# Performance work log

Hardware: AMD Instinct MI355X
Metric: run time of the kernel (lower is better)

The kernel has to match this reference:

```python
import jax, jax.numpy as jnp
import numpy as np

M0, M1 = 16, 8            # scalar / vector multiplicities of node_irreps (16x0e + 8x1o)
N_NODES = 10000
N_EDGES = 160000
H_EDGE = 64
W_NUMEL = M0*M0 + M1*M0 + M0*M1 + M1*M1  # 576 per-edge TP weights
EPS = 1e-5


def setup_inputs() -> dict:
    key = jax.random.key(0)
    ks = jax.random.split(key, 8)
    return {
        "node_features": jax.random.normal(ks[0], (N_NODES, M0 + 3*M1), jnp.float32),
        "edge_features": jax.random.normal(ks[1], (N_EDGES, H_EDGE), jnp.float32),
        "edge_sh": jax.random.normal(ks[2], (N_EDGES, 4), jnp.float32),
        "edge_index": jax.random.randint(ks[3], (2, N_EDGES), 0, N_NODES),
        "fc_w1": jax.random.normal(ks[4], (H_EDGE, H_EDGE), jnp.float32) / np.sqrt(H_EDGE),
        "fc_b1": jnp.zeros((H_EDGE,), jnp.float32),
        "fc_w2": jax.random.normal(ks[5], (H_EDGE, W_NUMEL), jnp.float32) / np.sqrt(H_EDGE),
        "fc_b2": jnp.zeros((W_NUMEL,), jnp.float32),
        "bn_w_s": jnp.ones((M0,), jnp.float32),
        "bn_b_s": jnp.zeros((M0,), jnp.float32),
        "bn_w_v": jnp.ones((M1,), jnp.float32),
    }


def reference(node_features, edge_features, edge_sh, edge_index,
              fc_w1, fc_b1, fc_w2, fc_b2, bn_w_s, bn_b_s, bn_w_v):
    N = node_features.shape[0]
    E = edge_features.shape[0]
    edge_dst, edge_src = edge_index[0], edge_index[1]

    # per-edge TP weights from a small MLP on edge features
    w = jax.nn.relu(edge_features @ fc_w1 + fc_b1) @ fc_w2 + fc_b2  # [E, 576]

    # gather node features on destination side
    x = node_features[edge_dst]                      # [E, 40]
    x0 = x[:, :M0]                                   # [E, 16] scalars (0e)
    x1 = x[:, M0:].reshape(E, M1, 3)                 # [E, 8, 3] vectors (1o)
    sh0 = edge_sh[:, 0]                              # [E] l=0
    sh1 = edge_sh[:, 1:4]                            # [E, 3] l=1

    # split per-edge weights by tensor-product path
    o1 = M0*M0; o2 = o1 + M1*M0; o3 = o2 + M0*M1
    w00 = w[:, :o1].reshape(E, M0, M0)               # 0e x 0e -> 0e
    w11 = w[:, o1:o2].reshape(E, M1, M0)             # 1o x 1o -> 0e
    w01 = w[:, o2:o3].reshape(E, M0, M1)             # 0e x 1o -> 1o
    w10 = w[:, o3:].reshape(E, M1, M1)               # 1o x 0e -> 1o

    inv3 = 1.0 / np.sqrt(3.0)                        # w3j(1,1,0) coefficient
    alpha = 1.0 / np.sqrt(M0 + M1)                   # path fan-in normalization

    out0 = (jnp.einsum('eu,euv->ev', x0 * sh0[:, None], w00)
            + inv3 * jnp.einsum('eui,ei,euv->ev', x1, sh1, w11)) * alpha   # [E, 16]
    out1 = (jnp.einsum('eu,ei,euv->evi', x0, sh1, w01)
            + jnp.einsum('e,eui,euv->evi', sh0, x1, w10)) * alpha          # [E, 8, 3]

    tp = jnp.concatenate([out0, out1.reshape(E, 3*M1)], axis=-1)           # [E, 40]

    # scatter_mean over source nodes
    seg = jax.ops.segment_sum(tp, edge_src, num_segments=N)                # [N, 40]
    cnt = jax.ops.segment_sum(jnp.ones((E, 1), tp.dtype), edge_src, num_segments=N)
    out = seg / jnp.maximum(cnt, 1.0)

    # residual (pad is zero-width since tp output irreps == node irreps)
    out = out + node_features

    # e3nn-style BatchNorm (training mode, component normalization)
    s = out[:, :M0]
    v = out[:, M0:].reshape(N, M1, 3)
    mu = s.mean(axis=0)
    s = s - mu
    var = (s * s).mean(axis=0)
    s = s * (jax.lax.rsqrt(var + EPS) * bn_w_s) + bn_b_s
    vnorm = (v * v).mean(axis=-1).mean(axis=0)       # [M1]
    v = v * (jax.lax.rsqrt(vnorm + EPS) * bn_w_v)[None, :, None]
    out = jnp.concatenate([s, v.reshape(N, 3*M1)], axis=-1)

    return out, edge_features
```

## Files before the change

### kernel.cpp

```cpp
#include <hip/hip_runtime.h>

typedef __attribute__((ext_vector_type(8))) short short8;
typedef __attribute__((ext_vector_type(4))) float f32x4;
typedef __attribute__((ext_vector_type(4))) ushort u16x4;

constexpr int NN = 10000;
constexpr int NE = 160000;
constexpr int NT = NE / 16;
constexpr int TPSTR = 48;
constexpr int GBLK = 625;
constexpr float EPSV = 1e-5f;
constexpr float INV3 = 0.57735026918962576f;
constexpr float ALPHA = 0.20412414523193152f;

__device__ __forceinline__ ushort f2bf(float x) {
  unsigned u = __float_as_uint(x);
  u += 0x7fffu + ((u >> 16) & 1u);
  return (ushort)(u >> 16);
}
__device__ __forceinline__ float bf2f(ushort u) {
  return __uint_as_float(((unsigned)u) << 16);
}
__device__ __forceinline__ f32x4 mfma16(short8 a, short8 b, f32x4 c) {
  return __builtin_amdgcn_mfma_f32_16x16x32_bf16(a, b, c, 0, 0, 0);
}

template <typename T> struct TPS;
template <> struct TPS<float> {
  static __device__ __forceinline__ void st4(float* p, f32x4 v) { *(f32x4*)p = v; }
  static __device__ __forceinline__ float ld(const float* p) { return *p; }
};
template <> struct TPS<ushort> {
  static __device__ __forceinline__ void st4(ushort* p, f32x4 v) {
    u16x4 o;
#pragma unroll
    for (int j = 0; j < 4; ++j) o[j] = f2bf(v[j]);
    *(u16x4*)p = o;
  }
  static __device__ __forceinline__ float ld(const ushort* p) { return bf2f(*p); }
};

constexpr int PREP_DEGB = (NN + 63) / 64;
__global__ __launch_bounds__(64) void prep_w2(const float* __restrict__ w2,
                                              short8* __restrict__ w2bf,
                                              int* __restrict__ deg,
                                              const float* __restrict__ b2,
                                              float* __restrict__ flag) {
  int b = blockIdx.x;
  int lane = threadIdx.x;
  if (b < 72) {
    int jt = b >> 1, kc = b & 1;
    int g = lane >> 4, c = lane & 15;
    short8 v;
#pragma unroll
    for (int j = 0; j < 8; ++j)
      v[j] = (short)f2bf(w2[(kc * 32 + 8 * g + j) * 576 + jt * 16 + c]);
    w2bf[(jt * 2 + kc) * 64 + lane] = v;
  } else if (b < 72 + PREP_DEGB) {
    int idx = (b - 72) * 64 + lane;
    if (idx < NN) deg[idx] = 0;
  } else {
    float m = 0.f;
    for (int i = lane; i < 576; i += 64) m = fmaxf(m, fabsf(b2[i]));
#pragma unroll
    for (int off = 1; off < 64; off <<= 1) m = fmaxf(m, __shfl_xor(m, off));
    if (lane == 0) *flag = m;
  }
}

constexpr int CSTR = 68;
constexpr unsigned SM_W2 = 4608 * 16;
constexpr unsigned SM_B2 = 576 * 4;
constexpr unsigned SM_W1 = 512 * 16;
constexpr unsigned SM_B1 = 64 * 4;
constexpr unsigned SM_HL = 8 * 16 * 72 * 2;
constexpr unsigned SM_SCR = 8 * 16 * CSTR * 4;
constexpr unsigned SM_TOTAL = SM_W2 + SM_B2 + SM_W1 + SM_B1 + SM_HL + SM_SCR;

template <typename T>
__global__ __launch_bounds__(512) void conv_kernel(
    const float* __restrict__ ef, const float* __restrict__ w1,
    const float* __restrict__ b1, const short8* __restrict__ w2bf,
    const float* __restrict__ b2, const float* __restrict__ nf,
    const float* __restrict__ sh, const int* __restrict__ ei,
    const int* __restrict__ perm, float* __restrict__ efout, int do_copy,
    T* __restrict__ tp, const float* __restrict__ flagp)
{
  extern __shared__ char smem[];
  short8* w2lds = (short8*)smem;
  float*  b2lds = (float*)(smem + SM_W2);
  short8* w1f   = (short8*)(smem + SM_W2 + SM_B2);
  float*  b1lds = (float*)(smem + SM_W2 + SM_B2 + SM_W1);
  ushort* hlall = (ushort*)(smem + SM_W2 + SM_B2 + SM_W1 + SM_B1);
  float*  scrall = (float*)(smem + SM_W2 + SM_B2 + SM_W1 + SM_B1 + SM_HL);

  const int tid = threadIdx.x;
  for (int i = tid; i < 4608; i += 512) w2lds[i] = w2bf[i];
  for (int i = tid; i < 576; i += 512) b2lds[i] = b2[i];
  {
    int tile = tid >> 6, l = tid & 63;
    int nt = tile >> 1, kc = tile & 1;
    int gg = l >> 4, cc = l & 15;
    short8 v;
#pragma unroll
    for (int j = 0; j < 8; ++j)
      v[j] = (short)f2bf(w1[(kc * 32 + 8 * gg + j) * 64 + nt * 16 + cc]);
    w1f[tid] = v;
  }
  if (tid < 64) b1lds[tid] = b1[tid];
  const bool nob2 = (*flagp == 0.f);
  __syncthreads();

  const int lane = tid & 63, wid = tid >> 6;
  const int g = lane >> 4, c = lane & 15;
  const int gh = g >> 1;
  const int e = lane >> 2, part = lane & 3;
  float* scr = scrall + wid * (16 * CSTR);
  ushort* hl = hlall + wid * (16 * 72);

  for (int t = blockIdx.x * 8 + wid; t < NT; t += gridDim.x * 8) {
    const int ege = t * 16 + e;
    const float* __restrict__ src = nf + (size_t)ei[ege] * 40;
    const f32x4 sv = *(const f32x4*)(sh + (size_t)ege * 4);
    const f32x4 v0 = *(const f32x4*)(src + part * 4);
    const f32x4 v1 = *(const f32x4*)(src + 16 + part * 4);
    f32x4 v2 = {};
    if (part < 2) v2 = *(const f32x4*)(src + 32 + part * 4);

    const long ebase = (long)t * 16;
    short8 af[2];
    const float* rowp = ef + (ebase + c) * 64;
#pragma unroll
    for (int kc = 0; kc < 2; ++kc) {
      const f32x4* p = (const f32x4*)(rowp + kc * 32 + 8 * g);
      f32x4 lo = p[0], hi = p[1];
      if (do_copy) {
        f32x4* q = (f32x4*)(efout + (ebase + c) * 64 + kc * 32 + 8 * g);
        q[0] = lo; q[1] = hi;
      }
      short8 v;
#pragma unroll
      for (int j = 0; j < 4; ++j) { v[j] = (short)f2bf(lo[j]); v[4 + j] = (short)f2bf(hi[j]); }
      af[kc] = v;
    }
    f32x4 hacc[4] = {};
#pragma unroll
    for (int nt = 0; nt < 4; ++nt)
#pragma unroll
      for (int kc = 0; kc < 2; ++kc)
        hacc[nt] = mfma16(af[kc], w1f[(nt * 2 + kc) * 64 + lane], hacc[nt]);

#pragma unroll
    for (int nt = 0; nt < 4; ++nt) {
      float bv = b1lds[nt * 16 + c];
#pragma unroll
      for (int q = 0; q < 4; ++q) {
        float h = fmaxf(hacc[nt][q] + bv, 0.f);
        hl[(4 * g + q) * 72 + nt * 16 + c] = f2bf(h);
      }
    }
    const short8 h0 = *(const short8*)&hl[c * 72 + 8 * g];
    const short8 h1 = *(const short8*)&hl[c * 72 + 32 + 8 * g];

    {
      float* ce = scr + e * CSTR;
      f32x4 a0;
#pragma unroll
      for (int q = 0; q < 4; ++q) a0[q] = sv[0] * v0[q];
      *(f32x4*)(ce + 4 * part) = a0;
      *(f32x4*)(ce + 24 + 4 * part) = v0;
      *(f32x4*)(ce + 40 + 4 * part) = v1;
      if (part < 2) *(f32x4*)(ce + 56 + 4 * part) = v2;
#pragma unroll
      for (int uu = 0; uu < 2; ++uu) {
        int u = 2 * part + uu;
        ce[16 + u] = INV3 * (ce[40 + 3 * u] * sv[1] + ce[41 + 3 * u] * sv[2] +
                             ce[42 + 3 * u] * sv[3]);
      }
    }
    const float* __restrict__ cc = scr + c * CSTR;

    f32x4 out0acc = {0.f, 0.f, 0.f, 0.f};
    f32x4 c0acc = {0.f, 0.f, 0.f, 0.f};
    f32x4 c1acc[3] = {};

    if (nob2) {
#pragma unroll
      for (int j4 = 0; j4 < 4; ++j4) {
        const f32x4 a4 = *(const f32x4*)&cc[j4 * 4];
#pragma unroll
        for (int jj = 0; jj < 4; ++jj) {
          const int jt = j4 * 4 + jj;
          f32x4 z = {0.f, 0.f, 0.f, 0.f};
          f32x4 d0 = mfma16(w2lds[(jt * 2 + 0) * 64 + lane], h0, z);
          f32x4 d1 = mfma16(w2lds[(jt * 2 + 1) * 64 + lane], h1, z);
          float a = a4[jj];
#pragma unroll
          for (int q = 0; q < 4; ++q) {
            out0acc[q] = fmaf(a, d0[q], out0acc[q]);
            out0acc[q] = fmaf(a, d1[q], out0acc[q]);
          }
        }
      }
#pragma unroll
      for (int j4 = 0; j4 < 2; ++j4) {
        const f32x4 a4 = *(const f32x4*)&cc[16 + j4 * 4];
#pragma unroll
        for (int jj = 0; jj < 4; ++jj) {
          const int jt = 16 + j4 * 4 + jj;
          f32x4 z = {0.f, 0.f, 0.f, 0.f};
          f32x4 d0 = mfma16(w2lds[(jt * 2 + 0) * 64 + lane], h0, z);
          f32x4 d1 = mfma16(w2lds[(jt * 2 + 1) * 64 + lane], h1, z);
          float a = a4[jj];
#pragma unroll
          for (int q = 0; q < 4; ++q) {
            out0acc[q] = fmaf(a, d0[q], out0acc[q]);
            out0acc[q] = fmaf(a, d1[q], out0acc[q]);
          }
        }
      }
#pragma unroll
      for (int jt = 24; jt < 32; ++jt) {
        f32x4 z = {0.f, 0.f, 0.f, 0.f};
        f32x4 d0 = mfma16(w2lds[(jt * 2 + 0) * 64 + lane], h0, z);
        f32x4 d1 = mfma16(w2lds[(jt * 2 + 1) * 64 + lane], h1, z);
        float a = cc[24 + 2 * (jt - 24) + gh];
#pragma unroll
        for (int q = 0; q < 4; ++q) {
          c0acc[q] = fmaf(a, d0[q], c0acc[q]);
          c0acc[q] = fmaf(a, d1[q], c0acc[q]);
        }
      }
#pragma unroll
      for (int jt = 32; jt < 36; ++jt) {
        f32x4 z = {0.f, 0.f, 0.f, 0.f};
        f32x4 d0 = mfma16(w2lds[(jt * 2 + 0) * 64 + lane], h0, z);
        f32x4 d1 = mfma16(w2lds[(jt * 2 + 1) * 64 + lane], h1, z);
        const int ub = 40 + 3 * (2 * (jt - 32) + gh);
#pragma unroll
        for (int i = 0; i < 3; ++i) {
          float a = cc[ub + i];
#pragma unroll
          for (int q = 0; q < 4; ++q) {
            c1acc[i][q] = fmaf(a, d0[q], c1acc[i][q]);
            c1acc[i][q] = fmaf(a, d1[q], c1acc[i][q]);
          }
        }
      }
    } else {
#pragma unroll
      for (int jt = 0; jt < 16; ++jt) {
        f32x4 d = *(const f32x4*)&b2lds[jt * 16 + 4 * g];
        d = mfma16(w2lds[(jt * 2 + 0) * 64 + lane], h0, d);
        d = mfma16(w2lds[(jt * 2 + 1) * 64 + lane], h1, d);
        float a = cc[jt];
#pragma unroll
        for (int q = 0; q < 4; ++q) out0acc[q] = fmaf(a, d[q], out0acc[q]);
      }
#pragma unroll
      for (int jt = 16; jt < 24; ++jt) {
        f32x4 d = *(const f32x4*)&b2lds[jt * 16 + 4 * g];
        d = mfma16(w2lds[(jt * 2 + 0) * 64 + lane], h0, d);
        d = mfma16(w2lds[(jt * 2 + 1) * 64 + lane], h1, d);
        float a = cc[16 + (jt - 16)];
#pragma unroll
        for (int q = 0; q < 4; ++q) out0acc[q] = fmaf(a, d[q], out0acc[q]);
      }
#pragma unroll
      for (int jt = 24; jt < 32; ++jt) {
        f32x4 d = *(const f32x4*)&b2lds[jt * 16 + 4 * g];
        d = mfma16(w2lds[(jt * 2 + 0) * 64 + lane], h0, d);
        d = mfma16(w2lds[(jt * 2 + 1) * 64 + lane], h1, d);
        float a = cc[24 + 2 * (jt - 24) + gh];
#pragma unroll
        for (int q = 0; q < 4; ++q) c0acc[q] = fmaf(a, d[q], c0acc[q]);
      }
#pragma unroll
      for (int jt = 32; jt < 36; ++jt) {
        f32x4 d = *(const f32x4*)&b2lds[jt * 16 + 4 * g];
        d = mfma16(w2lds[(jt * 2 + 0) * 64 + lane], h0, d);
        d = mfma16(w2lds[(jt * 2 + 1) * 64 + lane], h1, d);
        const int ub = 40 + 3 * (2 * (jt - 32) + gh);
#pragma unroll
        for (int i = 0; i < 3; ++i) {
          float a = cc[ub + i];
#pragma unroll
          for (int q = 0; q < 4; ++q) c1acc[i][q] = fmaf(a, d[q], c1acc[i][q]);
        }
      }
    }

#pragma unroll
    for (int q = 0; q < 4; ++q) c0acc[q] += __shfl_xor(c0acc[q], 32);
#pragma unroll
    for (int i = 0; i < 3; ++i)
#pragma unroll
      for (int q = 0; q < 4; ++q) c1acc[i][q] += __shfl_xor(c1acc[i][q], 32);

    const int eg = t * 16 + c;
    const f32x4 shv = *(const f32x4*)(sh + (size_t)eg * 4);
    T* tpr = tp + (size_t)perm[eg] * TPSTR;
    f32x4 o0;
#pragma unroll
    for (int q = 0; q < 4; ++q) o0[q] = ALPHA * out0acc[q];
    TPS<T>::st4(tpr + 4 * g, o0);
    if (g < 2) {
      float wv[12];
#pragma unroll
      for (int q = 0; q < 4; ++q)
#pragma unroll
        for (int i = 0; i < 3; ++i)
          wv[q * 3 + i] = ALPHA * (shv[1 + i] * c0acc[q] + shv[0] * c1acc[i][q]);
#pragma unroll
      for (int p = 0; p < 3; ++p) {
        f32x4 v = {wv[4 * p], wv[4 * p + 1], wv[4 * p + 2], wv[4 * p + 3]};
        TPS<T>::st4(tpr + 16 + 12 * g + 4 * p, v);
      }
    }
  }
}

__global__ __launch_bounds__(256) void hist_kernel(const int* __restrict__ ei,
                                                   int* __restrict__ deg) {
  for (int e = blockIdx.x * 256 + threadIdx.x; e < NE; e += gridDim.x * 256)
    atomicAdd(&deg[ei[NE + e]], 1);
}

__global__ __launch_bounds__(1024) void scan_kernel(const int* __restrict__ deg,
                                                    int* __restrict__ rowoff,
                                                    int* __restrict__ wcur) {
  __shared__ int s[1024];
  int t = threadIdx.x;
  int base = t * 10;
  int sum = 0;
#pragma unroll
  for (int j = 0; j < 10; ++j) { int n = base + j; sum += (n < NN) ? deg[n] : 0; }
  s[t] = sum;
  __syncthreads();
  for (int off = 1; off < 1024; off <<= 1) {
    int v = (t >= off) ? s[t - off] : 0;
    __syncthreads();
    s[t] += v;
    __syncthreads();
  }
  int run = s[t] - sum;
#pragma unroll
  for (int j = 0; j < 10; ++j) {
    int n = base + j;
    if (n < NN) { rowoff[n] = run; wcur[n] = run; run += deg[n]; }
  }
  if (t == 1023) rowoff[NN] = s[1023];
}

__global__ __launch_bounds__(256) void fill_kernel(const int* __restrict__ ei,
                                                   int* __restrict__ wcur,
                                                   int* __restrict__ perm) {
  for (int e = blockIdx.x * 256 + threadIdx.x; e < NE; e += gridDim.x * 256) {
    int pos = atomicAdd(&wcur[ei[NE + e]], 1);
    perm[e] = pos;
  }
}

template <typename T>
__global__ __launch_bounds__(256) void gather_kernel(
    const T* __restrict__ tp, const int* __restrict__ rowoff,
    const float* __restrict__ nf, float* __restrict__ pre,
    float* __restrict__ pstats)
{
  __shared__ float ls[40];
  const int tid = threadIdx.x;
  if (tid < 40) ls[tid] = 0.f;
  __syncthreads();
  const int wid = tid >> 6, lane = tid & 63;
  float sacc = 0.f, qacc = 0.f;
  if (lane < 40) {
#pragma unroll 1
    for (int i = 0; i < 4; ++i) {
      const int n = blockIdx.x * 16 + wid * 4 + i;
      const int r0 = rowoff[n], r1 = rowoff[n + 1];
      float s0 = 0.f, s1 = 0.f, s2 = 0.f, s3 = 0.f,
            s4 = 0.f, s5 = 0.f, s6 = 0.f, s7 = 0.f;
      int k = r0;
      for (; k + 8 <= r1; k += 8) {
        s0 += TPS<T>::ld(tp + (size_t)(k + 0) * TPSTR + lane);
        s1 += TPS<T>::ld(tp + (size_t)(k + 1) * TPSTR + lane);
        s2 += TPS<T>::ld(tp + (size_t)(k + 2) * TPSTR + lane);
        s3 += TPS<T>::ld(tp + (size_t)(k + 3) * TPSTR + lane);
        s4 += TPS<T>::ld(tp + (size_t)(k + 4) * TPSTR + lane);
        s5 += TPS<T>::ld(tp + (size_t)(k + 5) * TPSTR + lane);
        s6 += TPS<T>::ld(tp + (size_t)(k + 6) * TPSTR + lane);
        s7 += TPS<T>::ld(tp + (size_t)(k + 7) * TPSTR + lane);
      }
      for (; k < r1; ++k) s0 += TPS<T>::ld(tp + (size_t)k * TPSTR + lane);
      float s = ((s0 + s1) + (s2 + s3)) + ((s4 + s5) + (s6 + s7));
      float val = s / fmaxf((float)(r1 - r0), 1.f) + nf[(size_t)n * 40 + lane];
      pre[(size_t)n * 40 + lane] = val;
      if (lane < 16) { sacc += val; qacc += val * val; }
      else qacc += val * val;
    }
    if (lane < 16) {
      atomicAdd(&ls[lane], sacc);
      atomicAdd(&ls[16 + lane], qacc);
    } else {
      atomicAdd(&ls[32 + (lane - 16) / 3], qacc);
    }
  }
  __syncthreads();
  if (tid < 40) pstats[(size_t)blockIdx.x * 40 + tid] = ls[tid];
}

__global__ __launch_bounds__(256) void stats_reduce(
    const float* __restrict__ pstats, float* __restrict__ stats)
{
  const int c = blockIdx.x;
  float s = 0.f;
  for (int i = threadIdx.x; i < GBLK; i += 256) s += pstats[(size_t)i * 40 + c];
#pragma unroll
  for (int off = 1; off < 64; off <<= 1) s += __shfl_xor(s, off);
  __shared__ float red[4];
  if ((threadIdx.x & 63) == 0) red[threadIdx.x >> 6] = s;
  __syncthreads();
  if (threadIdx.x == 0) stats[c] = (red[0] + red[1]) + (red[2] + red[3]);
}

__global__ __launch_bounds__(256) void node_pass2(
    const float* __restrict__ pre, const float* __restrict__ stats,
    const float* __restrict__ bnws, const float* __restrict__ bnbs,
    const float* __restrict__ bnwv, float* __restrict__ out)
{
  int idx = blockIdx.x * blockDim.x + threadIdx.x;
  if (idx >= NN * 40) return;
  int n = idx / 40;
  int c = idx - n * 40;
  float val = pre[idx];
  constexpr float invN = 1.0f / NN;
  if (c < 16) {
    float mu = stats[c] * invN;
    float var = stats[16 + c] * invN - mu * mu;
    out[idx] = (val - mu) * (rsqrtf(var + EPSV) * bnws[c]) + bnbs[c];
  } else {
    int u = (c - 16) / 3;
    float vn = stats[32 + u] * (invN / 3.0f);
    out[idx] = val * (rsqrtf(vn + EPSV) * bnwv[u]);
  }
}

__global__ __launch_bounds__(256) void copy_ef(const f32x4* __restrict__ src,
                                               f32x4* __restrict__ dst) {
  const int n4 = NE * 64 / 4;
  for (int i = blockIdx.x * blockDim.x + threadIdx.x; i < n4;
       i += gridDim.x * blockDim.x)
    dst[i] = src[i];
}

extern "C" void kernel_launch(void* const* d_in, const int* in_sizes, int n_in,
                              void* d_out, int out_size, void* d_ws, size_t ws_size,
                              hipStream_t stream) {
  (void)in_sizes; (void)n_in; (void)out_size;
  const float* nf   = (const float*)d_in[0];
  const float* ef   = (const float*)d_in[1];
  const float* sh   = (const float*)d_in[2];
  const int*   ei   = (const int*)d_in[3];
  const float* w1   = (const float*)d_in[4];
  const float* b1   = (const float*)d_in[5];
  const float* w2   = (const float*)d_in[6];
  const float* b2   = (const float*)d_in[7];
  const float* bnws = (const float*)d_in[8];
  const float* bnbs = (const float*)d_in[9];
  const float* bnwv = (const float*)d_in[10];

  float* out = (float*)d_out;
  float* efout = out + (size_t)NN * 40;

  char* w = (char*)d_ws;
  int* deg     = (int*)w;
  float* stats = (float*)(w + (size_t)NN * 4);
  float* flag  = stats + 44;
  int* rowoff  = (int*)(w + (size_t)NN * 4 + 192);
  int* wcur    = rowoff + NN + 1;
  int* perm    = wcur + NN;
  float* pre   = (float*)(perm + NE);
  float* pstats = pre + (size_t)NN * 40;
  size_t base  = ((size_t)((char*)(pstats + (size_t)GBLK * 40) - w) + 255) & ~(size_t)255;
  short8* w2bf = (short8*)(w + base);
  size_t tpoff = (base + SM_W2 + 255) & ~(size_t)255;

  const size_t TPB_F32 = (size_t)NE * TPSTR * 4;
  const size_t needA = tpoff + TPB_F32;

  hipFuncSetAttribute((const void*)conv_kernel<float>,
                      hipFuncAttributeMaxDynamicSharedMemorySize, SM_TOTAL);
  hipFuncSetAttribute((const void*)conv_kernel<ushort>,
                      hipFuncAttributeMaxDynamicSharedMemorySize, SM_TOTAL);

  prep_w2<<<72 + PREP_DEGB + 1, 64, 0, stream>>>(w2, w2bf, deg, b2, flag);

  const int pblocks = (NN * 40 + 255) / 256;

  hist_kernel<<<625, 256, 0, stream>>>(ei, deg);
  scan_kernel<<<1, 1024, 0, stream>>>(deg, rowoff, wcur);
  fill_kernel<<<625, 256, 0, stream>>>(ei, wcur, perm);

  if (ws_size >= needA) {
    float* tp = (float*)(w + tpoff);
    conv_kernel<float><<<256, 512, SM_TOTAL, stream>>>(
        ef, w1, b1, w2bf, b2, nf, sh, ei, perm, efout, 1, tp, flag);
    gather_kernel<float><<<GBLK, 256, 0, stream>>>(tp, rowoff, nf, pre, pstats);
    stats_reduce<<<40, 256, 0, stream>>>(pstats, stats);
    node_pass2<<<pblocks, 256, 0, stream>>>(pre, stats, bnws, bnbs, bnwv, out);
  } else {
    ushort* tp = (ushort*)efout;
    conv_kernel<ushort><<<256, 512, SM_TOTAL, stream>>>(
        ef, w1, b1, w2bf, b2, nf, sh, ei, perm, efout, 0, tp, flag);
    gather_kernel<ushort><<<GBLK, 256, 0, stream>>>(tp, rowoff, nf, pre, pstats);
    stats_reduce<<<40, 256, 0, stream>>>(pstats, stats);
    node_pass2<<<pblocks, 256, 0, stream>>>(pre, stats, bnws, bnbs, bnwv, out);
    copy_ef<<<2048, 256, 0, stream>>>((const f32x4*)ef, (f32x4*)efout);
  }
}
```

Before: 98.02 us.

## Store per-edge TP intermediates in bf16 always and use wave-shuffle scan

Drops the fp32 tp buffer path so the conv kernel always writes bf16 per-edge outputs with a 64-element (128-byte) row stride, and the gather kernel reads bf16. This halves the bytes per row in the scatter-write and gather-read traffic that dominate the edge pipeline, and aligns each row to a cache line. The single-block scan is rewritten to use wave shuffles plus a small shared array instead of a 1024-entry Hillis-Steele loop with many barriers. The cost is bf16 rounding of every edge contribution before the mean aggregation, which lowers accuracy.

```diff
diff --git a/kernel.cpp b/kernel.cpp
--- a/kernel.cpp
+++ b/kernel.cpp
@@ -7,7 +7,7 @@
 constexpr int NN = 10000;
 constexpr int NE = 160000;
 constexpr int NT = NE / 16;
-constexpr int TPSTR = 48;
+constexpr int TPSTR = 64;
 constexpr int GBLK = 625;
 constexpr float EPSV = 1e-5f;
 constexpr float INV3 = 0.57735026918962576f;
@@ -24,21 +24,12 @@
 __device__ __forceinline__ f32x4 mfma16(short8 a, short8 b, f32x4 c) {
   return __builtin_amdgcn_mfma_f32_16x16x32_bf16(a, b, c, 0, 0, 0);
 }
-
-template <typename T> struct TPS;
-template <> struct TPS<float> {
-  static __device__ __forceinline__ void st4(float* p, f32x4 v) { *(f32x4*)p = v; }
-  static __device__ __forceinline__ float ld(const float* p) { return *p; }
-};
-template <> struct TPS<ushort> {
-  static __device__ __forceinline__ void st4(ushort* p, f32x4 v) {
-    u16x4 o;
-#pragma unroll
-    for (int j = 0; j < 4; ++j) o[j] = f2bf(v[j]);
-    *(u16x4*)p = o;
-  }
-  static __device__ __forceinline__ float ld(const ushort* p) { return bf2f(*p); }
-};
+__device__ __forceinline__ void st4u(ushort* p, f32x4 v) {
+  u16x4 o;
+#pragma unroll
+  for (int j = 0; j < 4; ++j) o[j] = f2bf(v[j]);
+  *(u16x4*)p = o;
+}
 
 constexpr int PREP_DEGB = (NN + 63) / 64;
 __global__ __launch_bounds__(64) void prep_w2(const float* __restrict__ w2,
@@ -77,14 +68,13 @@
 constexpr unsigned SM_SCR = 8 * 16 * CSTR * 4;
 constexpr unsigned SM_TOTAL = SM_W2 + SM_B2 + SM_W1 + SM_B1 + SM_HL + SM_SCR;
 
-template <typename T>
 __global__ __launch_bounds__(512) void conv_kernel(
     const float* __restrict__ ef, const float* __restrict__ w1,
     const float* __restrict__ b1, const short8* __restrict__ w2bf,
     const float* __restrict__ b2, const float* __restrict__ nf,
     const float* __restrict__ sh, const int* __restrict__ ei,
     const int* __restrict__ perm, float* __restrict__ efout, int do_copy,
-    T* __restrict__ tp, const float* __restrict__ flagp)
+    ushort* __restrict__ tp, const float* __restrict__ flagp)
 {
   extern __shared__ char smem[];
   short8* w2lds = (short8*)smem;
@@ -299,11 +289,11 @@
 
     const int eg = t * 16 + c;
     const f32x4 shv = *(const f32x4*)(sh + (size_t)eg * 4);
-    T* tpr = tp + (size_t)perm[eg] * TPSTR;
+    ushort* tpr = tp + (size_t)perm[eg] * TPSTR;
     f32x4 o0;
 #pragma unroll
     for (int q = 0; q < 4; ++q) o0[q] = ALPHA * out0acc[q];
-    TPS<T>::st4(tpr + 4 * g, o0);
+    st4u(tpr + 4 * g, o0);
     if (g < 2) {
       float wv[12];
 #pragma unroll
@@ -314,7 +304,7 @@
 #pragma unroll
       for (int p = 0; p < 3; ++p) {
         f32x4 v = {wv[4 * p], wv[4 * p + 1], wv[4 * p + 2], wv[4 * p + 3]};
-        TPS<T>::st4(tpr + 16 + 12 * g + 4 * p, v);
+        st4u(tpr + 16 + 12 * g + 4 * p, v);
       }
     }
   }
@@ -329,27 +319,45 @@
 __global__ __launch_bounds__(1024) void scan_kernel(const int* __restrict__ deg,
                                                     int* __restrict__ rowoff,
                                                     int* __restrict__ wcur) {
-  __shared__ int s[1024];
-  int t = threadIdx.x;
-  int base = t * 10;
+  __shared__ int wsum[16];
+  const int t = threadIdx.x;
+  const int lane = t & 63, wid = t >> 6;
+  const int base = t * 10;
+  int d[10];
   int sum = 0;
-#pragma unroll
-  for (int j = 0; j < 10; ++j) { int n = base + j; sum += (n < NN) ? deg[n] : 0; }
-  s[t] = sum;
-  __syncthreads();
-  for (int off = 1; off < 1024; off <<= 1) {
-    int v = (t >= off) ? s[t - off] : 0;
-    __syncthreads();
-    s[t] += v;
-    __syncthreads();
-  }
-  int run = s[t] - sum;
 #pragma unroll
   for (int j = 0; j < 10; ++j) {
     int n = base + j;
-    if (n < NN) { rowoff[n] = run; wcur[n] = run; run += deg[n]; }
-  }
-  if (t == 1023) rowoff[NN] = s[1023];
+    d[j] = (n < NN) ? deg[n] : 0;
+    sum += d[j];
+  }
+  int val = sum;
+#pragma unroll
+  for (int off = 1; off < 64; off <<= 1) {
+    int v = __shfl_up(val, off);
+    if (lane >= off) val += v;
+  }
+  if (lane == 63) wsum[wid] = val;
+  __syncthreads();
+  if (t < 16) {
+    int v = wsum[t];
+#pragma unroll
+    for (int off = 1; off < 16; off <<= 1) {
+      int u = __shfl_up(v, off);
+      if (t >= off) v += u;
+    }
+    wsum[t] = v;
+  }
+  __syncthreads();
+  const int waveoff = (wid > 0) ? wsum[wid - 1] : 0;
+  int run = waveoff + (val - sum);
+#pragma unroll
+  for (int j = 0; j < 10; ++j) {
+    int n = base + j;
+    if (n < NN) { rowoff[n] = run; wcur[n] = run; }
+    run += d[j];
+  }
+  if (t == 1023) rowoff[NN] = run;
 }
 
 __global__ __launch_bounds__(256) void fill_kernel(const int* __restrict__ ei,
@@ -361,9 +369,8 @@
   }
 }
 
-template <typename T>
 __global__ __launch_bounds__(256) void gather_kernel(
-    const T* __restrict__ tp, const int* __restrict__ rowoff,
+    const ushort* __restrict__ tp, const int* __restrict__ rowoff,
     const float* __restrict__ nf, float* __restrict__ pre,
     float* __restrict__ pstats)
 {
@@ -382,16 +389,16 @@
             s4 = 0.f, s5 = 0.f, s6 = 0.f, s7 = 0.f;
       int k = r0;
       for (; k + 8 <= r1; k += 8) {
-        s0 += TPS<T>::ld(tp + (size_t)(k + 0) * TPSTR + lane);
-        s1 += TPS<T>::ld(tp + (size_t)(k + 1) * TPSTR + lane);
-        s2 += TPS<T>::ld(tp + (size_t)(k + 2) * TPSTR + lane);
-        s3 += TPS<T>::ld(tp + (size_t)(k + 3) * TPSTR + lane);
-        s4 += TPS<T>::ld(tp + (size_t)(k + 4) * TPSTR + lane);
-        s5 += TPS<T>::ld(tp + (size_t)(k + 5) * TPSTR + lane);
-        s6 += TPS<T>::ld(tp + (size_t)(k + 6) * TPSTR + lane);
-        s7 += TPS<T>::ld(tp + (size_t)(k + 7) * TPSTR + lane);
-      }
-      for (; k < r1; ++k) s0 += TPS<T>::ld(tp + (size_t)k * TPSTR + lane);
+        s0 += bf2f(tp[(size_t)(k + 0) * TPSTR + lane]);
+        s1 += bf2f(tp[(size_t)(k + 1) * TPSTR + lane]);
+        s2 += bf2f(tp[(size_t)(k + 2) * TPSTR + lane]);
+        s3 += bf2f(tp[(size_t)(k + 3) * TPSTR + lane]);
+        s4 += bf2f(tp[(size_t)(k + 4) * TPSTR + lane]);
+        s5 += bf2f(tp[(size_t)(k + 5) * TPSTR + lane]);
+        s6 += bf2f(tp[(size_t)(k + 6) * TPSTR + lane]);
+        s7 += bf2f(tp[(size_t)(k + 7) * TPSTR + lane]);
+      }
+      for (; k < r1; ++k) s0 += bf2f(tp[(size_t)k * TPSTR + lane]);
       float s = ((s0 + s1) + (s2 + s3)) + ((s4 + s5) + (s6 + s7));
       float val = s / fmaxf((float)(r1 - r0), 1.f) + nf[(size_t)n * 40 + lane];
       pre[(size_t)n * 40 + lane] = val;
@@ -485,12 +492,10 @@
   short8* w2bf = (short8*)(w + base);
   size_t tpoff = (base + SM_W2 + 255) & ~(size_t)255;
 
-  const size_t TPB_F32 = (size_t)NE * TPSTR * 4;
-  const size_t needA = tpoff + TPB_F32;
-
-  hipFuncSetAttribute((const void*)conv_kernel<float>,
-                      hipFuncAttributeMaxDynamicSharedMemorySize, SM_TOTAL);
-  hipFuncSetAttribute((const void*)conv_kernel<ushort>,
+  const size_t TPB = (size_t)NE * TPSTR * 2;
+  const size_t needA = tpoff + TPB;
+
+  hipFuncSetAttribute((const void*)conv_kernel,
                       hipFuncAttributeMaxDynamicSharedMemorySize, SM_TOTAL);
 
   prep_w2<<<72 + PREP_DEGB + 1, 64, 0, stream>>>(w2, w2bf, deg, b2, flag);
@@ -502,17 +507,17 @@
   fill_kernel<<<625, 256, 0, stream>>>(ei, wcur, perm);
 
   if (ws_size >= needA) {
-    float* tp = (float*)(w + tpoff);
-    conv_kernel<float><<<256, 512, SM_TOTAL, stream>>>(
+    ushort* tp = (ushort*)(w + tpoff);
+    conv_kernel<<<256, 512, SM_TOTAL, stream>>>(
         ef, w1, b1, w2bf, b2, nf, sh, ei, perm, efout, 1, tp, flag);
-    gather_kernel<float><<<GBLK, 256, 0, stream>>>(tp, rowoff, nf, pre, pstats);
+    gather_kernel<<<GBLK, 256, 0, stream>>>(tp, rowoff, nf, pre, pstats);
     stats_reduce<<<40, 256, 0, stream>>>(pstats, stats);
     node_pass2<<<pblocks, 256, 0, stream>>>(pre, stats, bnws, bnbs, bnwv, out);
   } else {
     ushort* tp = (ushort*)efout;
-    conv_kernel<ushort><<<256, 512, SM_TOTAL, stream>>>(
+    conv_kernel<<<256, 512, SM_TOTAL, stream>>>(
         ef, w1, b1, w2bf, b2, nf, sh, ei, perm, efout, 0, tp, flag);
-    gather_kernel<ushort><<<GBLK, 256, 0, stream>>>(tp, rowoff, nf, pre, pstats);
+    gather_kernel<<<GBLK, 256, 0, stream>>>(tp, rowoff, nf, pre, pstats);
     stats_reduce<<<40, 256, 0, stream>>>(pstats, stats);
     node_pass2<<<pblocks, 256, 0, stream>>>(pre, stats, bnws, bnbs, bnwv, out);
     copy_ef<<<2048, 256, 0, stream>>>((const f32x4*)ef, (f32x4*)efout);
```

New measurement: 94.87 us (median of 2 runs). -3.2%, faster.
